# Kernel tuning notes

Hardware: AMD Instinct MI355X
Metric: run time of the kernel (lower is better)

## Reference

```python
import jax, jax.numpy as jnp
import numpy as np

WIDTH = 128


def setup_inputs() -> dict:
    key = jax.random.key(0)
    k_logits, k_w1, k_b1, k_w2, k_b2 = jax.random.split(key, 5)
    B, T, V = 32, 256, 4096
    logits = jax.random.normal(k_logits, (B, T, V), dtype=jnp.float32)
    # Linear(1, width): weight [width, 1] -> stored transposed as [1, width]
    w1 = jax.random.normal(k_w1, (1, WIDTH), dtype=jnp.float32) / jnp.sqrt(1.0)
    b1 = jax.random.normal(k_b1, (WIDTH,), dtype=jnp.float32) * 0.1
    # Linear(width, 1): weight [1, width] -> stored transposed as [width, 1]
    w2 = jax.random.normal(k_w2, (WIDTH, 1), dtype=jnp.float32) / jnp.sqrt(WIDTH)
    b2 = jax.random.normal(k_b2, (1,), dtype=jnp.float32) * 0.1
    return {"logits": logits, "w1": w1, "b1": b1, "w2": w2, "b2": b2}


def reference(logits, w1, b1, w2, b2):
    B, T, V = logits.shape
    logits_trim = logits[:, :-1, :]                       # [B, T-1, V]
    # entropy of softmax over the class dim; logits - logsumexp == log_softmax
    logp = jax.nn.log_softmax(logits_trim, axis=-1)       # [B, T-1, V]
    p = jnp.exp(logp)
    entropy = -jnp.sum(p * logp, axis=-1, keepdims=True)  # [B, T-1, 1]
    entropy_max = jnp.log(jnp.asarray(T, dtype=logits.dtype))  # log(num_steps)
    norm = 2.0 * entropy / entropy_max - 1.0              # [B, T-1, 1]
    # tiny 1 -> width -> 1 MLP
    hidden = jax.nn.relu(norm @ w1 + b1)                  # [B, T-1, width]
    lin = (2.0 * hidden) @ w2 + b2                        # [B, T-1, 1]
    # ns = [T-1, T-2, ..., 1]
    ns = jnp.arange(T - 1, 0, -1, dtype=logits.dtype).reshape(1, T - 1, 1)
    flags_trim = jax.nn.sigmoid(lin - jnp.log(ns))        # [B, T-1, 1]
    zeros = jnp.zeros((B, 1, 1), dtype=logits.dtype)
    ones = jnp.ones((B, 1, 1), dtype=logits.dtype)
    flags = jnp.concatenate([zeros, flags_trim, ones], axis=1)  # [B, T+1, 1]
    probabilities = jax.nn.softmax(logits, axis=2)        # [B, T, V]
    residuals = jnp.cumprod(1.0 - flags[:, :-1], axis=1)  # [B, T, 1] survival
    frequencies = probabilities * flags[:, 1:] * residuals  # [B, T, V]
    return frequencies
```

## Files before the change

kernel.cpp:

```cpp
#include <hip/hip_runtime.h>
#include <math.h>

#define T_DIM 256
#define V_DIM 4096
#define WIDTH 128

typedef float floatx4 __attribute__((ext_vector_type(4)));

__device__ __forceinline__ double wave_sum_d(double v) {
#pragma unroll
  for (int o = 32; o > 0; o >>= 1) v += __shfl_xor(v, o);
  return v;
}

__global__ __launch_bounds__(256) void row_stats(
    const float* __restrict__ logits,
    const float* __restrict__ w1, const float* __restrict__ b1,
    const float* __restrict__ w2, const float* __restrict__ b2,
    double* __restrict__ row_Z, double* __restrict__ row_flag) {
  const int row = blockIdx.x;
  const int t = row & (T_DIM - 1);
  const int tid = threadIdx.x;
  const int lane = tid & 63;
  const int wave = tid >> 6;

  const float4* src = (const float4*)(logits + (size_t)row * V_DIM);

  float z = 0.f, s = 0.f;
#pragma unroll
  for (int k = 0; k < 4; ++k) {
    float4 x = src[tid + k * 256];
    float vals[4] = {x.x, x.y, x.z, x.w};
#pragma unroll
    for (int j = 0; j < 4; ++j) {
      float ev = expf(vals[j]);
      z += ev;
      s = fmaf(vals[j], ev, s);
    }
  }
  double zd = wave_sum_d((double)z);
  double sd = wave_sum_d((double)s);

  __shared__ double szs[4], sss[4];
  __shared__ double sZ, sS;
  if (lane == 0) { szs[wave] = zd; sss[wave] = sd; }
  __syncthreads();

  if (tid == 0) {
    double zt = szs[0] + szs[1] + szs[2] + szs[3];
    double st = sss[0] + sss[1] + sss[2] + sss[3];
    sZ = zt; sS = st;
    row_Z[row] = zt;
  }
  __syncthreads();

  if (wave == 0 && t < T_DIM - 1) {
    double H = log(sZ) - sS / sZ;
    double nrm = 2.0 * H / log(256.0) - 1.0;
    double acc = 0.0;
#pragma unroll
    for (int j = lane; j < WIDTH; j += 64) {
      double h = fma(nrm, (double)w1[j], (double)b1[j]);
      h = h > 0.0 ? h : 0.0;
      acc = fma(h, (double)w2[j], acc);
    }
    acc = wave_sum_d(acc);
    if (lane == 0) {
      double lin = 2.0 * acc + (double)b2[0];
      double xx = lin - log((double)(T_DIM - 1 - t));
      row_flag[row] = 1.0 / (1.0 + exp(-xx));
    }
  }
}

__global__ __launch_bounds__(256) void out_k(const float* __restrict__ logits,
                                             const double* __restrict__ row_Z,
                                             const double* __restrict__ row_flag,
                                             float* __restrict__ out) {
  const int row = blockIdx.x;
  const int b = row >> 8;
  const int t0 = row & (T_DIM - 1);
  const int tid = threadIdx.x;
  const int lane = tid & 63;
  const int wave = tid >> 6;

  const float4* src = (const float4*)(logits + (size_t)row * V_DIM);
  floatx4* dst = (floatx4*)(out + (size_t)row * V_DIM);

  float4 x[4];
#pragma unroll
  for (int k = 0; k < 4; ++k) x[k] = src[tid + k * 256];

  __shared__ float sScale;
  __shared__ double fl[T_DIM];
  if (wave == 0) {
    const double* fb = row_flag + (size_t)b * T_DIM;
#pragma unroll
    for (int j = lane; j < T_DIM; j += 64)
      fl[j] = (j == T_DIM - 1) ? 1.0 : fb[j];

    double loc[4];
    double p = 1.0;
#pragma unroll
    for (int j = 0; j < 4; ++j) {
      int t = lane * 4 + j;
      double flag_t = (t == 0) ? 0.0 : fl[t - 1];
      p *= (1.0 - flag_t);
      loc[j] = p;
    }
    double inc = p;
#pragma unroll
    for (int o = 1; o < 64; o <<= 1) {
      double up = __shfl_up(inc, o);
      if (lane >= o) inc *= up;
    }
    double exc = __shfl_up(inc, 1);
    if (lane == 0) exc = 1.0;

    if (lane == (t0 >> 2)) {
      double resid = exc * loc[t0 & 3];
      sScale = (float)(fl[t0] * resid / row_Z[row]);
    }
  }
  __syncthreads();
  const float sc = sScale;

#pragma unroll
  for (int k = 0; k < 4; ++k) {
    floatx4 o;
    o.x = expf(x[k].x) * sc;
    o.y = expf(x[k].y) * sc;
    o.z = expf(x[k].z) * sc;
    o.w = expf(x[k].w) * sc;
    __builtin_nontemporal_store(o, &dst[tid + k * 256]);
  }
}

extern "C" void kernel_launch(void* const* d_in, const int* in_sizes, int n_in,
                              void* d_out, int out_size, void* d_ws, size_t ws_size,
                              hipStream_t stream) {
  const float* logits = (const float*)d_in[0];
  const float* w1 = (const float*)d_in[1];
  const float* b1 = (const float*)d_in[2];
  const float* w2 = (const float*)d_in[3];
  const float* b2 = (const float*)d_in[4];
  float* out = (float*)d_out;

  const size_t nrows = (size_t)in_sizes[0] / V_DIM;

  double* row_Z = (double*)d_ws;
  double* row_flag = row_Z + nrows;

  row_stats<<<(int)nrows, 256, 0, stream>>>(logits, w1, b1, w2, b2, row_Z,
                                            row_flag);
  out_k<<<(int)nrows, 256, 0, stream>>>(logits, row_Z, row_flag, out);
}
```

Measured before the change: 253.3 us.

## Compute per-row scales via last-block-per-batch in stats kernel, slim output kernel

The per-batch cumulative product of survival terms moves out of every output block. It now runs once per batch in the last row_stats block to finish, detected with an atomic counter. The output kernel reads a single precomputed float scale per row and uses the fast __expf intrinsic. This removes the redundant 256-element scan and shared-memory sync from each output block. In exchange it adds a memset launch, atomics and fences, and __expf gives slightly lower accuracy.

```diff
diff --git a/kernel.cpp b/kernel.cpp
--- a/kernel.cpp
+++ b/kernel.cpp
@@ -17,8 +17,10 @@
     const float* __restrict__ logits,
     const float* __restrict__ w1, const float* __restrict__ b1,
     const float* __restrict__ w2, const float* __restrict__ b2,
-    double* __restrict__ row_Z, double* __restrict__ row_flag) {
+    double* __restrict__ row_Z, double* __restrict__ row_flag,
+    float* __restrict__ row_scale, unsigned int* __restrict__ cnt) {
   const int row = blockIdx.x;
+  const int b = row >> 8;
   const int t = row & (T_DIM - 1);
   const int tid = threadIdx.x;
   const int lane = tid & 63;
@@ -43,6 +45,7 @@
 
   __shared__ double szs[4], sss[4];
   __shared__ double sZ, sS;
+  __shared__ int sLast;
   if (lane == 0) { szs[wave] = zd; sss[wave] = sd; }
   __syncthreads();
 
@@ -71,30 +74,17 @@
       row_flag[row] = 1.0 / (1.0 + exp(-xx));
     }
   }
-}
 
-__global__ __launch_bounds__(256) void out_k(const float* __restrict__ logits,
-                                             const double* __restrict__ row_Z,
-                                             const double* __restrict__ row_flag,
-                                             float* __restrict__ out) {
-  const int row = blockIdx.x;
-  const int b = row >> 8;
-  const int t0 = row & (T_DIM - 1);
-  const int tid = threadIdx.x;
-  const int lane = tid & 63;
-  const int wave = tid >> 6;
+  if (tid == 0) {
+    __threadfence();
+    sLast = (atomicAdd(&cnt[b], 1u) == T_DIM - 1) ? 1 : 0;
+  }
+  __syncthreads();
 
-  const float4* src = (const float4*)(logits + (size_t)row * V_DIM);
-  floatx4* dst = (floatx4*)(out + (size_t)row * V_DIM);
-
-  float4 x[4];
-#pragma unroll
-  for (int k = 0; k < 4; ++k) x[k] = src[tid + k * 256];
-
-  __shared__ float sScale;
-  __shared__ double fl[T_DIM];
-  if (wave == 0) {
+  if (sLast && wave == 0) {
+    __threadfence();
     const double* fb = row_flag + (size_t)b * T_DIM;
+    __shared__ double fl[T_DIM];
 #pragma unroll
     for (int j = lane; j < T_DIM; j += 64)
       fl[j] = (j == T_DIM - 1) ? 1.0 : fb[j];
@@ -103,8 +93,8 @@
     double p = 1.0;
 #pragma unroll
     for (int j = 0; j < 4; ++j) {
-      int t = lane * 4 + j;
-      double flag_t = (t == 0) ? 0.0 : fl[t - 1];
+      int tt = lane * 4 + j;
+      double flag_t = (tt == 0) ? 0.0 : fl[tt - 1];
       p *= (1.0 - flag_t);
       loc[j] = p;
     }
@@ -117,21 +107,34 @@
     double exc = __shfl_up(inc, 1);
     if (lane == 0) exc = 1.0;
 
-    if (lane == (t0 >> 2)) {
-      double resid = exc * loc[t0 & 3];
-      sScale = (float)(fl[t0] * resid / row_Z[row]);
+#pragma unroll
+    for (int j = 0; j < 4; ++j) {
+      int tt = lane * 4 + j;
+      double resid = exc * loc[j];
+      row_scale[(size_t)b * T_DIM + tt] =
+          (float)(fl[tt] * resid / row_Z[(size_t)b * T_DIM + tt]);
     }
   }
-  __syncthreads();
-  const float sc = sScale;
+}
+
+__global__ __launch_bounds__(256) void out_k(const float* __restrict__ logits,
+                                             const float* __restrict__ row_scale,
+                                             float* __restrict__ out) {
+  const int row = blockIdx.x;
+  const int tid = threadIdx.x;
+  const float sc = row_scale[row];
+
+  const float4* src = (const float4*)(logits + (size_t)row * V_DIM);
+  floatx4* dst = (floatx4*)(out + (size_t)row * V_DIM);
 
 #pragma unroll
   for (int k = 0; k < 4; ++k) {
+    float4 x = src[tid + k * 256];
     floatx4 o;
-    o.x = expf(x[k].x) * sc;
-    o.y = expf(x[k].y) * sc;
-    o.z = expf(x[k].z) * sc;
-    o.w = expf(x[k].w) * sc;
+    o.x = __expf(x.x) * sc;
+    o.y = __expf(x.y) * sc;
+    o.z = __expf(x.z) * sc;
+    o.w = __expf(x.w) * sc;
     __builtin_nontemporal_store(o, &dst[tid + k * 256]);
   }
 }
@@ -147,11 +150,16 @@
   float* out = (float*)d_out;
 
   const size_t nrows = (size_t)in_sizes[0] / V_DIM;
+  const size_t nbatch = nrows / T_DIM;
 
   double* row_Z = (double*)d_ws;
   double* row_flag = row_Z + nrows;
+  float* row_scale = (float*)(row_flag + nrows);
+  unsigned int* cnt = (unsigned int*)(row_scale + nrows);
+
+  hipMemsetAsync(cnt, 0, nbatch * sizeof(unsigned int), stream);
 
   row_stats<<<(int)nrows, 256, 0, stream>>>(logits, w1, b1, w2, b2, row_Z,
-                                            row_flag);
-  out_k<<<(int)nrows, 256, 0, stream>>>(logits, row_Z, row_flag, out);
+                                            row_flag, row_scale, cnt);
+  out_k<<<(int)nrows, 256, 0, stream>>>(logits, row_scale, out);
 }
```

Result: slower. 529.4 us (+109.0%).
